# Kernel optimization log

Hardware: AMD Instinct MI355X
Metric: run time of the kernel (lower is better)

Reference implementation:

```python
import jax, jax.numpy as jnp
import numpy as np

B, T, C, H = 4, 2048, 1024, 16
D = C // H  # head_dim = 64

def setup_inputs() -> dict:
    key = jax.random.key(0)
    k1, k2, k3 = jax.random.split(key, 3)
    x = jax.random.normal(k1, (B, T, C), dtype=jnp.float32)
    W_attn = jax.random.normal(k2, (C, 3 * C), dtype=jnp.float32) * (C ** -0.5)
    b_attn = jnp.zeros((3 * C,), dtype=jnp.float32)
    W_proj = jax.random.normal(k3, (C, C), dtype=jnp.float32) * (C ** -0.5)
    b_proj = jnp.zeros((C,), dtype=jnp.float32)
    return {"x": x, "W_attn": W_attn, "b_attn": b_attn, "W_proj": W_proj, "b_proj": b_proj}

def reference(x, W_attn, b_attn, W_proj, b_proj):
    Bc, Tc, Cc = x.shape
    qkv = x @ W_attn + b_attn                       # [B,T,3C]
    q, k, v = jnp.split(qkv, 3, axis=-1)
    q = q.reshape(Bc, Tc, H, D).transpose(0, 2, 1, 3)  # [B,H,T,D]
    k = k.reshape(Bc, Tc, H, D).transpose(0, 2, 1, 3)
    v = v.reshape(Bc, Tc, H, D).transpose(0, 2, 1, 3)
    scores = jnp.einsum('bhqd,bhkd->bhqk', q, k) / jnp.sqrt(jnp.float32(D))
    causal = jnp.tril(jnp.ones((Tc, Tc), dtype=bool))
    scores = jnp.where(causal[None, None, :, :], scores, jnp.float32(-jnp.inf))
    wei = jax.nn.softmax(scores, axis=-1)           # dropout=0 -> identity
    out = jnp.einsum('bhqk,bhkd->bhqd', wei, v)     # [B,H,T,D]
    out = out.transpose(0, 2, 1, 3).reshape(Bc, Tc, Cc)
    return out @ W_proj + b_proj
```

## Files before the change

kernel.cpp:

```cpp
#include <hip/hip_runtime.h>
#include <cstdint>
#include <cstddef>

#define Bsz   4
#define Tsz   2048
#define Csz   1024
#define Hn    16
#define Dh    64
#define Mrows 8192
#define KD    1024

#define NEG_BIG (-1.0e30f)
#define SCL2  0.18033688011112042f
#define PBIAS (-11.541560327111707f)

typedef unsigned short u16;
typedef __bf16  bf16x8 __attribute__((ext_vector_type(8)));
typedef __bf16  bf16x2 __attribute__((ext_vector_type(2)));
typedef float   f32x4  __attribute__((ext_vector_type(4)));
typedef unsigned int u32x4 __attribute__((ext_vector_type(4)));

__device__ __forceinline__ u16 f2bf(float f) {
  union { float f; unsigned int i; } v; v.f = f;
  unsigned int u = v.i;
  return (u16)((u + 0x7fffu + ((u >> 16) & 1u)) >> 16);
}
__device__ __forceinline__ unsigned int pack2bf(float a, float b) {
#if __has_builtin(__builtin_amdgcn_cvt_pk_bf16_f32)
  union { bf16x2 h; unsigned int u; } cv;
  cv.h = __builtin_amdgcn_cvt_pk_bf16_f32(a, b);
  return cv.u;
#else
  return (unsigned int)f2bf(a) | ((unsigned int)f2bf(b) << 16);
#endif
}
__device__ __forceinline__ unsigned int pack2bf_trunc(float lo, float hi) {
  return __builtin_amdgcn_perm(__builtin_bit_cast(unsigned int, hi),
                               __builtin_bit_cast(unsigned int, lo),
                               0x07060302u);
}
__device__ __forceinline__ float fast_exp2(float x) {
#if __has_builtin(__builtin_amdgcn_exp2f)
  return __builtin_amdgcn_exp2f(x);
#else
  return exp2f(x);
#endif
}

__global__ __launch_bounds__(256)
void cvt_f32_bf16(const float* __restrict__ in, u16* __restrict__ out, int n4) {
  const int i = blockIdx.x * 256 + threadIdx.x;
  if (i >= n4) return;
  const float4 v = ((const float4*)in)[i];
  uint2 o;
  o.x = pack2bf(v.x, v.y);
  o.y = pack2bf(v.z, v.w);
  ((uint2*)out)[i] = o;
}

__global__ __launch_bounds__(256)
void transpose_f32_bf16(const float* __restrict__ in, u16* __restrict__ out,
                        int rows, int cols) {
  __shared__ u16 tile[64][65];
  const int tc = blockIdx.x * 64, tr = blockIdx.y * 64;
  const int x = threadIdx.x & 63, y0 = threadIdx.x >> 6;
#pragma unroll
  for (int yy = 0; yy < 64; yy += 4) {
    int r = yy + y0;
    tile[r][x] = f2bf(in[(size_t)(tr + r) * cols + tc + x]);
  }
  __syncthreads();
#pragma unroll
  for (int yy = 0; yy < 64; yy += 4) {
    int r = yy + y0;
    out[(size_t)(tc + r) * rows + tr + x] = tile[x][r];
  }
}

template<int MODE>
__global__ __launch_bounds__(256)
void gemm_bt(const u16* __restrict__ A, const u16* __restrict__ BT,
             const float* __restrict__ bias, u16* __restrict__ o0,
             u16* __restrict__ o1, u16* __restrict__ o2,
             float* __restrict__ fout, int N) {
  __shared__ u16 lsA[128 * 32];
  __shared__ u16 lsB[128 * 32];
  const int tid  = threadIdx.x;
  const int lane = tid & 63;
  const int wid  = tid >> 6;
  const int wm   = wid & 1, wn = wid >> 1;
  const int quad = lane >> 4, l15 = lane & 15;
  const int m0 = blockIdx.y * 128, n0 = blockIdx.x * 128;

  f32x4 acc[4][4];
#pragma unroll
  for (int i = 0; i < 4; ++i)
#pragma unroll
    for (int j = 0; j < 4; ++j) acc[i][j] = (f32x4){0.f, 0.f, 0.f, 0.f};

#if __has_builtin(__builtin_amdgcn_global_load_lds)
  const int srow = lane >> 2, schunk = lane & 3;
  const u16* gA = A  + (size_t)(m0 + wid * 32 + srow) * KD + schunk * 8;
  const u16* gB = BT + (size_t)(n0 + wid * 32 + srow) * KD + schunk * 8;
  u16* lA0 = &lsA[(wid * 32) * 32];
  u16* lB0 = &lsB[(wid * 32) * 32];
#endif

  for (int kk = 0; kk < KD; kk += 32) {
#if __has_builtin(__builtin_amdgcn_global_load_lds)
#pragma unroll
    for (int i = 0; i < 2; ++i) {
      __builtin_amdgcn_global_load_lds(
          (const __attribute__((address_space(1))) void*)(gA + (size_t)i * 16 * KD + kk),
          (__attribute__((address_space(3))) void*)(lA0 + i * 16 * 32), 16, 0, 0);
      __builtin_amdgcn_global_load_lds(
          (const __attribute__((address_space(1))) void*)(gB + (size_t)i * 16 * KD + kk),
          (__attribute__((address_space(3))) void*)(lB0 + i * 16 * 32), 16, 0, 0);
    }
#else
#pragma unroll
    for (int cc = 0; cc < 2; ++cc) {
      int c = tid + cc * 256;
      int row = c >> 2, ch = c & 3;
      *(uint4*)&lsA[row * 32 + ch * 8] =
          *(const uint4*)&A[(size_t)(m0 + row) * KD + kk + ch * 8];
      *(uint4*)&lsB[row * 32 + ch * 8] =
          *(const uint4*)&BT[(size_t)(n0 + row) * KD + kk + ch * 8];
    }
#endif
    __syncthreads();
    bf16x8 af[4], bfv[4];
#pragma unroll
    for (int i = 0; i < 4; ++i)
      af[i] = *(const bf16x8*)&lsA[(wm * 64 + i * 16 + l15) * 32 + quad * 8];
#pragma unroll
    for (int j = 0; j < 4; ++j)
      bfv[j] = *(const bf16x8*)&lsB[(wn * 64 + j * 16 + l15) * 32 + quad * 8];
#pragma unroll
    for (int i = 0; i < 4; ++i)
#pragma unroll
      for (int j = 0; j < 4; ++j)
        acc[i][j] = __builtin_amdgcn_mfma_f32_16x16x32_bf16(af[i], bfv[j],
                                                            acc[i][j], 0, 0, 0);
    __syncthreads();
  }

#pragma unroll
  for (int i = 0; i < 4; ++i) {
#pragma unroll
    for (int j = 0; j < 4; ++j) {
      const int colb = n0 + wn * 64 + j * 16 + l15;
      const float bv = bias[colb];
      float vals[4];
#pragma unroll
      for (int r = 0; r < 4; ++r) vals[r] = acc[i][j][r] + bv;
      const int row0 = m0 + wm * 64 + i * 16 + quad * 4;
      if (MODE == 0) {
        const int b = row0 >> 11, t0 = row0 & (Tsz - 1);
        const int region = colb >> 10;
        const int nc = colb & (Csz - 1);
        const int h = nc >> 6, d = nc & 63;
        if (region == 2) {
          uint2 st;
          st.x = pack2bf(vals[0], vals[1]);
          st.y = pack2bf(vals[2], vals[3]);
          *(uint2*)&o2[((size_t)((b << 4) + h) * Dh + d) * Tsz + t0] = st;
        } else {
          u16* dst = (region == 0) ? o0 : o1;
#pragma unroll
          for (int r = 0; r < 4; ++r)
            dst[(size_t)(((b << 4) + h) * Tsz + t0 + r) * Dh + d] = f2bf(vals[r]);
        }
      } else {
#pragma unroll
        for (int r = 0; r < 4; ++r)
          fout[(size_t)(row0 + r) * N + colb] = vals[r];
      }
    }
  }
}

__global__ __launch_bounds__(256)
void attn_fused(const u16* __restrict__ qb, const u16* __restrict__ kbuf,
                const u16* __restrict__ vT, u16* __restrict__ outp) {
  __shared__ u16 Kl[64 * 72];
  __shared__ u16 Vt[64 * 72];
  const int tid = threadIdx.x, lane = tid & 63, w = tid >> 6;
  const int quad = lane >> 4, l15 = lane & 15;
  const int bh = blockIdx.x;
  const int b = bh >> 4, h = bh & 15;
  const u16* Q   = qb   + (size_t)bh * Tsz * Dh;
  const u16* Kg  = kbuf + (size_t)bh * Tsz * Dh;
  const u16* VTg = vT   + (size_t)bh * Dh * Tsz;

  for (int ph = 0; ph < 2; ++ph) {
    const int jq = ph ? (int)blockIdx.y : 31 - (int)blockIdx.y;

    const int qrow = jq * 64 + w * 16 + l15;
    const bf16x8 bq0 = *(const bf16x8*)&Q[(size_t)qrow * Dh + quad * 8];
    const bf16x8 bq1 = *(const bf16x8*)&Q[(size_t)qrow * Dh + 32 + quad * 8];

    f32x4 O[4];
#pragma unroll
    for (int nb = 0; nb < 4; ++nb) O[nb] = (f32x4){0.f, 0.f, 0.f, 0.f};
    float l_i = 0.f;

    for (int j = 0; j <= jq; ++j) {
      const int kb = j * 64;
#pragma unroll
      for (int cc = 0; cc < 2; ++cc) {
        const int c = tid + cc * 256;
        const int rr = c >> 3, off = c & 7;
        *(uint4*)&Kl[rr * 72 + off * 8] =
            *(const uint4*)&Kg[(size_t)(kb + rr) * Dh + off * 8];
        *(uint4*)&Vt[rr * 72 + off * 8] =
            *(const uint4*)&VTg[(size_t)rr * Tsz + kb + off * 8];
      }
      __syncthreads();

      const bool diag = (j == jq);
      const int tmax = diag ? (w + 1) : 4;

      f32x4 S[4];
#pragma unroll
      for (int t = 0; t < 4; ++t) S[t] = (f32x4){0.f, 0.f, 0.f, 0.f};
#pragma unroll
      for (int t = 0; t < 4; ++t) {
        if (t < tmax) {
          bf16x8 ak = *(const bf16x8*)&Kl[(t * 16 + l15) * 72 + quad * 8];
          S[t] = __builtin_amdgcn_mfma_f32_16x16x32_bf16(ak, bq0, S[t], 0, 0, 0);
          ak = *(const bf16x8*)&Kl[(t * 16 + l15) * 72 + 32 + quad * 8];
          S[t] = __builtin_amdgcn_mfma_f32_16x16x32_bf16(ak, bq1, S[t], 0, 0, 0);
        }
      }

      float p[4][4];
      if (diag) {
#pragma unroll
        for (int t = 0; t < 4; ++t) {
          const int key0 = kb + t * 16 + quad * 4;
#pragma unroll
          for (int r = 0; r < 4; ++r) {
            const float sv =
                (t < tmax && key0 + r <= qrow) ? S[t][r] : NEG_BIG;
            p[t][r] = fast_exp2(__builtin_fmaf(sv, SCL2, PBIAS));
            l_i += p[t][r];
          }
        }
      } else {
#pragma unroll
        for (int t = 0; t < 4; ++t)
#pragma unroll
          for (int r = 0; r < 4; ++r) {
            p[t][r] = fast_exp2(__builtin_fmaf(S[t][r], SCL2, PBIAS));
            l_i += p[t][r];
          }
      }

      u32x4 pu;
      pu[0] = pack2bf_trunc(p[0][0], p[0][1]);
      pu[1] = pack2bf_trunc(p[0][2], p[0][3]);
      pu[2] = pack2bf_trunc(p[1][0], p[1][1]);
      pu[3] = pack2bf_trunc(p[1][2], p[1][3]);
      bf16x8 pb = __builtin_bit_cast(bf16x8, pu);
#pragma unroll
      for (int nb = 0; nb < 4; ++nb) {
        const uint2 a0 = *(const uint2*)&Vt[(nb * 16 + l15) * 72 + quad * 4];
        const uint2 a1 = *(const uint2*)&Vt[(nb * 16 + l15) * 72 + 16 + quad * 4];
        const u32x4 au = {a0.x, a0.y, a1.x, a1.y};
        O[nb] = __builtin_amdgcn_mfma_f32_16x16x32_bf16(
            __builtin_bit_cast(bf16x8, au), pb, O[nb], 0, 0, 0);
      }
      if (tmax > 2) {
        pu[0] = pack2bf_trunc(p[2][0], p[2][1]);
        pu[1] = pack2bf_trunc(p[2][2], p[2][3]);
        pu[2] = pack2bf_trunc(p[3][0], p[3][1]);
        pu[3] = pack2bf_trunc(p[3][2], p[3][3]);
        pb = __builtin_bit_cast(bf16x8, pu);
#pragma unroll
        for (int nb = 0; nb < 4; ++nb) {
          const uint2 a0 = *(const uint2*)&Vt[(nb * 16 + l15) * 72 + 32 + quad * 4];
          const uint2 a1 = *(const uint2*)&Vt[(nb * 16 + l15) * 72 + 48 + quad * 4];
          const u32x4 au = {a0.x, a0.y, a1.x, a1.y};
          O[nb] = __builtin_amdgcn_mfma_f32_16x16x32_bf16(
              __builtin_bit_cast(bf16x8, au), pb, O[nb], 0, 0, 0);
        }
      }
      __syncthreads();
    }

    float lt = l_i + __shfl_xor(l_i, 16, 64);
    lt += __shfl_xor(lt, 32, 64);
    const float inv = 1.0f / lt;
#pragma unroll
    for (int nb = 0; nb < 4; ++nb) {
      uint2 st;
      st.x = pack2bf(O[nb][0] * inv, O[nb][1] * inv);
      st.y = pack2bf(O[nb][2] * inv, O[nb][3] * inv);
      *(uint2*)&outp[(size_t)(b * Tsz + qrow) * Csz + h * Dh + nb * 16 + quad * 4] = st;
    }
  }
}

extern "C" void kernel_launch(void* const* d_in, const int* in_sizes, int n_in,
                              void* d_out, int out_size, void* d_ws, size_t ws_size,
                              hipStream_t stream) {
  const float* x      = (const float*)d_in[0];
  const float* W_attn = (const float*)d_in[1];
  const float* b_attn = (const float*)d_in[2];
  const float* W_proj = (const float*)d_in[3];
  const float* b_proj = (const float*)d_in[4];
  float* out = (float*)d_out;

  u16* ws   = (u16*)d_ws;
  u16* xbf  = ws;
  u16* qbuf = xbf  + (size_t)Mrows * Csz;
  u16* kbuf = qbuf + (size_t)Mrows * Csz;
  u16* vbuf = kbuf + (size_t)Mrows * Csz;
  u16* aout = vbuf + (size_t)Mrows * Csz;
  u16* WTa  = aout + (size_t)Mrows * Csz;
  u16* WTp  = WTa  + (size_t)Csz * 3 * Csz;

  cvt_f32_bf16<<<(Mrows * Csz / 4 + 255) / 256, 256, 0, stream>>>(
      x, xbf, Mrows * Csz / 4);
  transpose_f32_bf16<<<dim3(3 * Csz / 64, Csz / 64), 256, 0, stream>>>(
      W_attn, WTa, Csz, 3 * Csz);
  transpose_f32_bf16<<<dim3(Csz / 64, Csz / 64), 256, 0, stream>>>(
      W_proj, WTp, Csz, Csz);
  gemm_bt<0><<<dim3(3 * Csz / 128, Mrows / 128), 256, 0, stream>>>(
      xbf, WTa, b_attn, qbuf, kbuf, vbuf, nullptr, 3 * Csz);
  attn_fused<<<dim3(Bsz * Hn, Tsz / 128), 256, 0, stream>>>(
      qbuf, kbuf, vbuf, aout);
  gemm_bt<1><<<dim3(Csz / 128, Mrows / 128), 256, 0, stream>>>(
      aout, WTp, b_proj, nullptr, nullptr, nullptr, out, Csz);
}
```

Baseline: 267.4 us.

## Restructure attention to 2-wave blocks with two query tiles per wave

The attention kernel moves from 4 waves per block, each with one 16-row query tile and a two-phase balanced loop, to 2 waves per block, each holding two 16-row query tiles that share every K and V LDS fragment load. The grid now launches one block per 64-row query tile instead of pairing tiles for load balance. V is stored into LDS in a permuted order so each PV fragment comes from a single 16-byte read. The aim is fewer LDS reads per MFMA and more blocks in flight, at the cost of more registers per wave and a less balanced causal workload across blocks.

```diff
diff --git a/kernel.cpp b/kernel.cpp
--- a/kernel.cpp
+++ b/kernel.cpp
@@ -180,7 +180,7 @@
   }
 }
 
-__global__ __launch_bounds__(256)
+__global__ __launch_bounds__(128, 4)
 void attn_fused(const u16* __restrict__ qb, const u16* __restrict__ kbuf,
                 const u16* __restrict__ vT, u16* __restrict__ outp) {
   __shared__ u16 Kl[64 * 72];
@@ -188,117 +188,154 @@
   const int tid = threadIdx.x, lane = tid & 63, w = tid >> 6;
   const int quad = lane >> 4, l15 = lane & 15;
   const int bh = blockIdx.x;
+  const int jq = 31 - blockIdx.y;
   const int b = bh >> 4, h = bh & 15;
   const u16* Q   = qb   + (size_t)bh * Tsz * Dh;
   const u16* Kg  = kbuf + (size_t)bh * Tsz * Dh;
   const u16* VTg = vT   + (size_t)bh * Dh * Tsz;
 
-  for (int ph = 0; ph < 2; ++ph) {
-    const int jq = ph ? (int)blockIdx.y : 31 - (int)blockIdx.y;
-
-    const int qrow = jq * 64 + w * 16 + l15;
-    const bf16x8 bq0 = *(const bf16x8*)&Q[(size_t)qrow * Dh + quad * 8];
-    const bf16x8 bq1 = *(const bf16x8*)&Q[(size_t)qrow * Dh + 32 + quad * 8];
-
-    f32x4 O[4];
-#pragma unroll
-    for (int nb = 0; nb < 4; ++nb) O[nb] = (f32x4){0.f, 0.f, 0.f, 0.f};
-    float l_i = 0.f;
-
-    for (int j = 0; j <= jq; ++j) {
-      const int kb = j * 64;
-#pragma unroll
-      for (int cc = 0; cc < 2; ++cc) {
-        const int c = tid + cc * 256;
-        const int rr = c >> 3, off = c & 7;
-        *(uint4*)&Kl[rr * 72 + off * 8] =
-            *(const uint4*)&Kg[(size_t)(kb + rr) * Dh + off * 8];
-        *(uint4*)&Vt[rr * 72 + off * 8] =
-            *(const uint4*)&VTg[(size_t)rr * Tsz + kb + off * 8];
-      }
-      __syncthreads();
-
-      const bool diag = (j == jq);
-      const int tmax = diag ? (w + 1) : 4;
-
-      f32x4 S[4];
-#pragma unroll
-      for (int t = 0; t < 4; ++t) S[t] = (f32x4){0.f, 0.f, 0.f, 0.f};
+  const int qrowA = jq * 64 + w * 32 + l15;
+  const int qrowB = qrowA + 16;
+  const bf16x8 bqA0 = *(const bf16x8*)&Q[(size_t)qrowA * Dh + quad * 8];
+  const bf16x8 bqA1 = *(const bf16x8*)&Q[(size_t)qrowA * Dh + 32 + quad * 8];
+  const bf16x8 bqB0 = *(const bf16x8*)&Q[(size_t)qrowB * Dh + quad * 8];
+  const bf16x8 bqB1 = *(const bf16x8*)&Q[(size_t)qrowB * Dh + 32 + quad * 8];
+
+  f32x4 OA[4], OB[4];
+#pragma unroll
+  for (int nb = 0; nb < 4; ++nb) {
+    OA[nb] = (f32x4){0.f, 0.f, 0.f, 0.f};
+    OB[nb] = (f32x4){0.f, 0.f, 0.f, 0.f};
+  }
+  float lA = 0.f, lB = 0.f;
+
+  for (int j = 0; j <= jq; ++j) {
+    const int kb = j * 64;
+#pragma unroll
+    for (int cc = 0; cc < 4; ++cc) {
+      const int c = tid + cc * 128;
+      const int rr = c >> 3, off = c & 7;
+      *(uint4*)&Kl[rr * 72 + off * 8] =
+          *(const uint4*)&Kg[(size_t)(kb + rr) * Dh + off * 8];
+      const uint4 vv = *(const uint4*)&VTg[(size_t)rr * Tsz + kb + off * 8];
+      const int g0 = off * 2, g1 = off * 2 + 1;
+      uint2 st0; st0.x = vv.x; st0.y = vv.y;
+      uint2 st1; st1.x = vv.z; st1.y = vv.w;
+      *(uint2*)&Vt[rr * 72 + ((g0 >> 3) * 32 + (g0 & 3) * 8 + ((g0 >> 2) & 1) * 4)] = st0;
+      *(uint2*)&Vt[rr * 72 + ((g1 >> 3) * 32 + (g1 & 3) * 8 + ((g1 >> 2) & 1) * 4)] = st1;
+    }
+    __syncthreads();
+
+    const bool diag = (j == jq);
+    const int tmaxA = diag ? (2 * w + 1) : 4;
+    const int tmaxB = diag ? (2 * w + 2) : 4;
+
+    f32x4 SA[4], SB[4];
+#pragma unroll
+    for (int t = 0; t < 4; ++t) {
+      SA[t] = (f32x4){0.f, 0.f, 0.f, 0.f};
+      SB[t] = (f32x4){0.f, 0.f, 0.f, 0.f};
+    }
+#pragma unroll
+    for (int t = 0; t < 4; ++t) {
+      if (t < tmaxB) {
+        const bf16x8 ak0 = *(const bf16x8*)&Kl[(t * 16 + l15) * 72 + quad * 8];
+        const bf16x8 ak1 = *(const bf16x8*)&Kl[(t * 16 + l15) * 72 + 32 + quad * 8];
+        if (t < tmaxA) {
+          SA[t] = __builtin_amdgcn_mfma_f32_16x16x32_bf16(ak0, bqA0, SA[t], 0, 0, 0);
+          SA[t] = __builtin_amdgcn_mfma_f32_16x16x32_bf16(ak1, bqA1, SA[t], 0, 0, 0);
+        }
+        SB[t] = __builtin_amdgcn_mfma_f32_16x16x32_bf16(ak0, bqB0, SB[t], 0, 0, 0);
+        SB[t] = __builtin_amdgcn_mfma_f32_16x16x32_bf16(ak1, bqB1, SB[t], 0, 0, 0);
+      }
+    }
+
+    float pA[4][4], pB[4][4];
+    if (diag) {
 #pragma unroll
       for (int t = 0; t < 4; ++t) {
-        if (t < tmax) {
-          bf16x8 ak = *(const bf16x8*)&Kl[(t * 16 + l15) * 72 + quad * 8];
-          S[t] = __builtin_amdgcn_mfma_f32_16x16x32_bf16(ak, bq0, S[t], 0, 0, 0);
-          ak = *(const bf16x8*)&Kl[(t * 16 + l15) * 72 + 32 + quad * 8];
-          S[t] = __builtin_amdgcn_mfma_f32_16x16x32_bf16(ak, bq1, S[t], 0, 0, 0);
+        const int key0 = kb + t * 16 + quad * 4;
+#pragma unroll
+        for (int r = 0; r < 4; ++r) {
+          if (t < tmaxA) {
+            const float sv = (key0 + r <= qrowA) ? SA[t][r] : NEG_BIG;
+            pA[t][r] = fast_exp2(__builtin_fmaf(sv, SCL2, PBIAS));
+            lA += pA[t][r];
+          } else pA[t][r] = 0.f;
+          if (t < tmaxB) {
+            const float sv = (key0 + r <= qrowB) ? SB[t][r] : NEG_BIG;
+            pB[t][r] = fast_exp2(__builtin_fmaf(sv, SCL2, PBIAS));
+            lB += pB[t][r];
+          } else pB[t][r] = 0.f;
         }
       }
-
-      float p[4][4];
-      if (diag) {
-#pragma unroll
-        for (int t = 0; t < 4; ++t) {
-          const int key0 = kb + t * 16 + quad * 4;
-#pragma unroll
-          for (int r = 0; r < 4; ++r) {
-            const float sv =
-                (t < tmax && key0 + r <= qrow) ? S[t][r] : NEG_BIG;
-            p[t][r] = fast_exp2(__builtin_fmaf(sv, SCL2, PBIAS));
-            l_i += p[t][r];
-          }
+    } else {
+#pragma unroll
+      for (int t = 0; t < 4; ++t)
+#pragma unroll
+        for (int r = 0; r < 4; ++r) {
+          pA[t][r] = fast_exp2(__builtin_fmaf(SA[t][r], SCL2, PBIAS));
+          lA += pA[t][r];
+          pB[t][r] = fast_exp2(__builtin_fmaf(SB[t][r], SCL2, PBIAS));
+          lB += pB[t][r];
         }
-      } else {
-#pragma unroll
-        for (int t = 0; t < 4; ++t)
-#pragma unroll
-          for (int r = 0; r < 4; ++r) {
-            p[t][r] = fast_exp2(__builtin_fmaf(S[t][r], SCL2, PBIAS));
-            l_i += p[t][r];
-          }
-      }
-
-      u32x4 pu;
-      pu[0] = pack2bf_trunc(p[0][0], p[0][1]);
-      pu[1] = pack2bf_trunc(p[0][2], p[0][3]);
-      pu[2] = pack2bf_trunc(p[1][0], p[1][1]);
-      pu[3] = pack2bf_trunc(p[1][2], p[1][3]);
-      bf16x8 pb = __builtin_bit_cast(bf16x8, pu);
+    }
+
+    {
+      u32x4 puA, puB;
+      puA[0] = pack2bf_trunc(pA[0][0], pA[0][1]);
+      puA[1] = pack2bf_trunc(pA[0][2], pA[0][3]);
+      puA[2] = pack2bf_trunc(pA[1][0], pA[1][1]);
+      puA[3] = pack2bf_trunc(pA[1][2], pA[1][3]);
+      puB[0] = pack2bf_trunc(pB[0][0], pB[0][1]);
+      puB[1] = pack2bf_trunc(pB[0][2], pB[0][3]);
+      puB[2] = pack2bf_trunc(pB[1][0], pB[1][1]);
+      puB[3] = pack2bf_trunc(pB[1][2], pB[1][3]);
+      const bf16x8 pbA = __builtin_bit_cast(bf16x8, puA);
+      const bf16x8 pbB = __builtin_bit_cast(bf16x8, puB);
 #pragma unroll
       for (int nb = 0; nb < 4; ++nb) {
-        const uint2 a0 = *(const uint2*)&Vt[(nb * 16 + l15) * 72 + quad * 4];
-        const uint2 a1 = *(const uint2*)&Vt[(nb * 16 + l15) * 72 + 16 + quad * 4];
-        const u32x4 au = {a0.x, a0.y, a1.x, a1.y};
-        O[nb] = __builtin_amdgcn_mfma_f32_16x16x32_bf16(
-            __builtin_bit_cast(bf16x8, au), pb, O[nb], 0, 0, 0);
-      }
-      if (tmax > 2) {
-        pu[0] = pack2bf_trunc(p[2][0], p[2][1]);
-        pu[1] = pack2bf_trunc(p[2][2], p[2][3]);
-        pu[2] = pack2bf_trunc(p[3][0], p[3][1]);
-        pu[3] = pack2bf_trunc(p[3][2], p[3][3]);
-        pb = __builtin_bit_cast(bf16x8, pu);
-#pragma unroll
-        for (int nb = 0; nb < 4; ++nb) {
-          const uint2 a0 = *(const uint2*)&Vt[(nb * 16 + l15) * 72 + 32 + quad * 4];
-          const uint2 a1 = *(const uint2*)&Vt[(nb * 16 + l15) * 72 + 48 + quad * 4];
-          const u32x4 au = {a0.x, a0.y, a1.x, a1.y};
-          O[nb] = __builtin_amdgcn_mfma_f32_16x16x32_bf16(
-              __builtin_bit_cast(bf16x8, au), pb, O[nb], 0, 0, 0);
-        }
-      }
-      __syncthreads();
-    }
-
-    float lt = l_i + __shfl_xor(l_i, 16, 64);
-    lt += __shfl_xor(lt, 32, 64);
-    const float inv = 1.0f / lt;
-#pragma unroll
-    for (int nb = 0; nb < 4; ++nb) {
-      uint2 st;
-      st.x = pack2bf(O[nb][0] * inv, O[nb][1] * inv);
-      st.y = pack2bf(O[nb][2] * inv, O[nb][3] * inv);
-      *(uint2*)&outp[(size_t)(b * Tsz + qrow) * Csz + h * Dh + nb * 16 + quad * 4] = st;
-    }
+        const bf16x8 av = *(const bf16x8*)&Vt[(nb * 16 + l15) * 72 + quad * 8];
+        OA[nb] = __builtin_amdgcn_mfma_f32_16x16x32_bf16(av, pbA, OA[nb], 0, 0, 0);
+        OB[nb] = __builtin_amdgcn_mfma_f32_16x16x32_bf16(av, pbB, OB[nb], 0, 0, 0);
+      }
+    }
+    if (tmaxB > 2) {
+      u32x4 puA, puB;
+      puA[0] = pack2bf_trunc(pA[2][0], pA[2][1]);
+      puA[1] = pack2bf_trunc(pA[2][2], pA[2][3]);
+      puA[2] = pack2bf_trunc(pA[3][0], pA[3][1]);
+      puA[3] = pack2bf_trunc(pA[3][2], pA[3][3]);
+      puB[0] = pack2bf_trunc(pB[2][0], pB[2][1]);
+      puB[1] = pack2bf_trunc(pB[2][2], pB[2][3]);
+      puB[2] = pack2bf_trunc(pB[3][0], pB[3][1]);
+      puB[3] = pack2bf_trunc(pB[3][2], pB[3][3]);
+      const bf16x8 pbA = __builtin_bit_cast(bf16x8, puA);
+      const bf16x8 pbB = __builtin_bit_cast(bf16x8, puB);
+#pragma unroll
+      for (int nb = 0; nb < 4; ++nb) {
+        const bf16x8 av = *(const bf16x8*)&Vt[(nb * 16 + l15) * 72 + 32 + quad * 8];
+        OA[nb] = __builtin_amdgcn_mfma_f32_16x16x32_bf16(av, pbA, OA[nb], 0, 0, 0);
+        OB[nb] = __builtin_amdgcn_mfma_f32_16x16x32_bf16(av, pbB, OB[nb], 0, 0, 0);
+      }
+    }
+    __syncthreads();
+  }
+
+  float ltA = lA + __shfl_xor(lA, 16, 64);
+  ltA += __shfl_xor(ltA, 32, 64);
+  float ltB = lB + __shfl_xor(lB, 16, 64);
+  ltB += __shfl_xor(ltB, 32, 64);
+  const float invA = 1.0f / ltA, invB = 1.0f / ltB;
+#pragma unroll
+  for (int nb = 0; nb < 4; ++nb) {
+    uint2 st;
+    st.x = pack2bf(OA[nb][0] * invA, OA[nb][1] * invA);
+    st.y = pack2bf(OA[nb][2] * invA, OA[nb][3] * invA);
+    *(uint2*)&outp[(size_t)(b * Tsz + qrowA) * Csz + h * Dh + nb * 16 + quad * 4] = st;
+    st.x = pack2bf(OB[nb][0] * invB, OB[nb][1] * invB);
+    st.y = pack2bf(OB[nb][2] * invB, OB[nb][3] * invB);
+    *(uint2*)&outp[(size_t)(b * Tsz + qrowB) * Csz + h * Dh + nb * 16 + quad * 4] = st;
   }
 }
 
@@ -329,7 +366,7 @@
       W_proj, WTp, Csz, Csz);
   gemm_bt<0><<<dim3(3 * Csz / 128, Mrows / 128), 256, 0, stream>>>(
       xbf, WTa, b_attn, qbuf, kbuf, vbuf, nullptr, 3 * Csz);
-  attn_fused<<<dim3(Bsz * Hn, Tsz / 128), 256, 0, stream>>>(
+  attn_fused<<<dim3(Bsz * Hn, Tsz / 64), 128, 0, stream>>>(
       qbuf, kbuf, vbuf, aout);
   gemm_bt<1><<<dim3(Csz / 128, Mrows / 128), 256, 0, stream>>>(
       aout, WTp, b_proj, nullptr, nullptr, nullptr, out, Csz);
```

Result: slower. 290.4 us (+8.6%).
